# Optimization experiments

Measured on AMD Instinct MI355X. Metric: run time of the kernel, lower is better.

## Reference

```python
import jax, jax.numpy as jnp
import numpy as np
from jax import lax

F8 = jnp.float8_e4m3fn


def setup_inputs() -> dict:
    key = jax.random.key(0)
    kx, kw = jax.random.split(key)
    x = jax.random.normal(kx, (2, 128, 4, 192, 320), dtype=jnp.float32)
    # matches reset_parameters: normal(0, 0.02) then cast to fp8
    weight = jax.random.normal(kw, (128, 128, 3, 3, 3), dtype=jnp.float32) * 0.02
    return {"x": x, "weight": weight}


def reference(x, weight):
    # fp8 e4m3 quantization round-trip (the torch module stores/consumes fp8),
    # compute/accumulate in fp32 as an fp8 conv kernel would.
    xq = x.astype(F8).astype(jnp.float32)
    wq = weight.astype(F8).astype(jnp.float32)
    # causal temporal padding: (kT-1, 0) = (2, 0); spatial 'same' padding (1,1)
    xp = jnp.pad(xq, ((0, 0), (0, 0), (2, 0), (1, 1), (1, 1)))
    out = lax.conv_general_dilated(
        xp, wq,
        window_strides=(1, 1, 1),
        padding='VALID',
        dimension_numbers=('NCDHW', 'OIDHW', 'NCDHW'),
    )  # (B, 128, 4, 192, 320)
    return out
```

## Files before the change

### kernel.cpp

```cpp
#include <hip/hip_runtime.h>
#include <hip/hip_fp8.h>


using f32x16 = __attribute__((ext_vector_type(16))) float;
using i32x8 = __attribute__((ext_vector_type(8))) int;
typedef long long i64;
struct alignas(16) L2v { i64 x, y; };

namespace {
constexpr int Cc = 128, Dd = 4, Hh = 192, Ww = 320;
constexpr int HP = 194, WP = 322;
constexpr int NTAP = 27;
constexpr size_t PLANE = (size_t)4 * WP * 32;
constexpr size_t XQ_BYTES = (size_t)2 * Dd * HP * PLANE;
constexpr int ZA = 8 * 2 * 2576;
constexpr int ZB = 8 * 192 * 32;
constexpr int GSTR = WP * 32;
}

__global__ __launch_bounds__(256) void zero_pad_kernel(unsigned char* __restrict__ xq) {
  int i = blockIdx.x * 256 + threadIdx.x;
  if (i < ZA) {
    int bd = i / (2 * 2576);
    int r = i - bd * (2 * 2576);
    int hsel = r / 2576, seg = r - hsel * 2576;
    L2v z{0, 0};
    *(L2v*)(xq + ((size_t)bd * HP + (hsel ? 193 : 0)) * PLANE + (size_t)seg * 16) = z;
  } else if (i < ZA + ZB) {
    int j = i - ZA;
    int bd = j / (192 * 32);
    int r = j - bd * (192 * 32);
    int h = r / 32 + 1;
    int t = r & 31;
    int g = t >> 3, s2 = t & 7;
    int wsel = s2 >> 2, part = s2 & 3;
    *(i64*)(xq + ((size_t)bd * HP + h) * PLANE + (size_t)g * GSTR
            + (size_t)(wsel ? 321 : 0) * 32 + part * 8) = 0;
  }
}

__global__ __launch_bounds__(256) void qx_kernel(const float* __restrict__ x,
                                                 unsigned char* __restrict__ xq) {
  __shared__ unsigned char lt[64 * 136];
  const int tid = threadIdx.x;
  const int b = blockIdx.z >> 2, d = blockIdx.z & 3;
  const int h = blockIdx.y;
  const int w0 = blockIdx.x * 64;
  const int wl = tid & 63, cig = tid >> 6;
  const size_t cstr = (size_t)Dd * Hh * Ww;
  const float* xp = x + (((size_t)b * Cc * Dd + d) * Hh + h) * Ww + w0 + wl;
  #pragma unroll 4
  for (int i = 0; i < 32; ++i) {
    int ci = cig * 32 + i;
    __hip_fp8_e4m3 q(xp[ci * cstr]);
    lt[wl * 136 + ci] = q.__x;
  }
  __syncthreads();
  unsigned char* plane = xq + ((size_t)(b * Dd + d) * HP + h + 1) * PLANE;
  {
    int g = tid >> 6, w = tid & 63;
    const unsigned char* src = lt + w * 136 + g * 32;
    i64 a0 = *(const i64*)(src), a1 = *(const i64*)(src + 8);
    i64 a2 = *(const i64*)(src + 16), a3 = *(const i64*)(src + 24);
    unsigned char* dst = plane + (size_t)g * GSTR + (size_t)(w0 + 1 + w) * 32;
    *(L2v*)dst = L2v{a0, a1};
    *(L2v*)(dst + 16) = L2v{a2, a3};
  }
}

__global__ void wpack_kernel(const float* __restrict__ w, unsigned char* __restrict__ wpk) {
  int idx = blockIdx.x * 256 + threadIdx.x;
  if (idx >= Cc * Cc * NTAP) return;
  int tap = idx % NTAP;
  int t = idx / NTAP;
  int ci = t % Cc, co = t / Cc;
  int cc = ci >> 6, cq = co >> 5;
  int lane = (((ci >> 5) & 1) << 5) | (co & 31);
  __hip_fp8_e4m3 q(w[idx]);
  wpk[((((size_t)tap * 2 + cc) * 4 + cq) * 64 + lane) * 32 + (ci & 31)] = q.__x;
}

__global__ __launch_bounds__(512, 4) void conv_mfma(const unsigned char* __restrict__ xq,
                                                    const unsigned char* __restrict__ wpk,
                                                    float* __restrict__ out) {
  __shared__ unsigned char lb[16 * 2112];
  const int tid = threadIdx.x;
  const int lane = tid & 63, wv = tid >> 6;
  const int l31 = lane & 31, chalf = lane >> 5;
  const int hr = wv >> 2, ch = wv & 3;
  const int id = blockIdx.x;
  const int xcd = id & 7, j = id >> 3;
  const int h0l = j / 40, rem = j - h0l * 40;
  const int z = rem / 5, wx = rem - z * 5;
  const int b = z >> 2, dout = z & 3;
  const int h0 = (xcd * 12 + h0l) * 2;
  const int w0 = wx * 64;
  const int kdmin = dout >= 2 ? 0 : 2 - dout;

  const unsigned char* bbl[3];
  const unsigned char* bbh[3];
  {
    unsigned char* rbase = lb + (hr * 4 + chalf) * 2112;
    #pragma unroll
    for (int kw = 0; kw < 3; ++kw) {
      int wl = l31 + kw;
      int t = (wl >> 2) & 1;
      bbl[kw] = rbase + 32 * wl + 16 * t;
      bbh[kw] = rbase + 32 * wl + 16 * (1 - t);
    }
  }

  f32x16 acc[2];
  #pragma unroll
  for (int n = 0; n < 2; ++n)
    #pragma unroll
    for (int r = 0; r < 16; ++r) acc[n][r] = 0.f;

  for (int kd = kdmin; kd < 3; ++kd) {
    __syncthreads();
    #pragma unroll
    for (int it = 0; it < 3; ++it) {
      int u = tid + it * 512;
      if (u < 1056) {
        int w = u % 66, rest = u / 66;
        int g = rest & 3, hrow = rest >> 2;
        const unsigned char* src = xq
            + ((size_t)(b * Dd + dout + kd - 2) * HP + h0 + hrow) * PLANE
            + (size_t)g * GSTR + (size_t)(w0 + w) * 32;
        L2v lo = *(const L2v*)src;
        L2v hi = *(const L2v*)(src + 16);
        int t = (w >> 2) & 1;
        unsigned char* base = lb + rest * 2112;
        *(L2v*)(base + (2 * w + t) * 16) = lo;
        *(L2v*)(base + (2 * w + 1 - t) * 16) = hi;
      }
    }
    __syncthreads();
    __builtin_amdgcn_s_setprio(1);
    #pragma unroll
    for (int kh = 0; kh < 3; ++kh)
      #pragma unroll
      for (int cc = 0; cc < 2; ++cc) {
        i32x8 av[3];
        #pragma unroll
        for (int kw = 0; kw < 3; ++kw) {
          const unsigned char* ap = wpk +
              ((((size_t)(kd * 9 + kh * 3 + kw) * 2 + cc) * 4 + ch) * 64 + lane) * 32;
          int4 alo = *(const int4*)ap;
          int4 ahi = *(const int4*)(ap + 16);
          av[kw][0] = alo.x; av[kw][1] = alo.y; av[kw][2] = alo.z; av[kw][3] = alo.w;
          av[kw][4] = ahi.x; av[kw][5] = ahi.y; av[kw][6] = ahi.z; av[kw][7] = ahi.w;
        }
        #pragma unroll
        for (int kw = 0; kw < 3; ++kw)
          #pragma unroll
          for (int nf = 0; nf < 2; ++nf) {
            const int off = (kh * 4 + cc * 2) * 2112 + nf * 1024;
            int4 blo = *(const int4*)(bbl[kw] + off);
            int4 bhi = *(const int4*)(bbh[kw] + off);
            i32x8 bv;
            bv[0] = blo.x; bv[1] = blo.y; bv[2] = blo.z; bv[3] = blo.w;
            bv[4] = bhi.x; bv[5] = bhi.y; bv[6] = bhi.z; bv[7] = bhi.w;
            acc[nf] = __builtin_amdgcn_mfma_scale_f32_32x32x64_f8f6f4(
                av[kw], bv, acc[nf], 0, 0, 0, 127, 0, 127);
          }
      }
    __builtin_amdgcn_s_setprio(0);
  }

  #pragma unroll
  for (int nf = 0; nf < 2; ++nf) {
    int ww = w0 + nf * 32 + l31;
    #pragma unroll
    for (int reg = 0; reg < 16; ++reg) {
      int co = ch * 32 + (reg & 3) + 8 * (reg >> 2) + 4 * chalf;
      out[(((size_t)b * Cc + co) * Dd + dout) * (size_t)(Hh * Ww)
          + (size_t)(h0 + hr) * Ww + ww] = acc[nf][reg];
    }
  }
}

extern "C" void kernel_launch(void* const* d_in, const int* in_sizes, int n_in,
                              void* d_out, int out_size, void* d_ws, size_t ws_size,
                              hipStream_t stream) {
  const float* x = (const float*)d_in[0];
  const float* w = (const float*)d_in[1];
  unsigned char* xq = (unsigned char*)d_ws;
  unsigned char* wpk = xq + XQ_BYTES;
  float* out = (float*)d_out;

  int nz = ZA + ZB;
  zero_pad_kernel<<<(nz + 255) / 256, 256, 0, stream>>>(xq);

  dim3 g1(Ww / 64, Hh, 2 * Dd);
  qx_kernel<<<g1, 256, 0, stream>>>(x, xq);

  int nw = Cc * Cc * NTAP;
  wpack_kernel<<<(nw + 255) / 256, 256, 0, stream>>>(w, wpk);

  conv_mfma<<<dim3(3840), 512, 0, stream>>>(xq, wpk, out);
}
```

Measured before the change: 238.4 us.

## Halve block to 4 waves with 64-channel output tiles per wave and split LDS layout

Each block now runs 256 threads (4 waves), and each wave computes two 32-channel output tiles. Every B fragment read from LDS therefore feeds two MFMAs, which halves LDS B reads per MFMA. The LDS layout changes from interleaved 32-byte pixels with a swizzle to separate low and high 16-byte halves placed HB bytes apart, which removes the swizzle arithmetic. The trade-offs are doubled accumulator registers per wave, fewer threads to stage each input tile, and a possible change in LDS bank-conflict behaviour.

```diff
diff --git a/kernel.cpp b/kernel.cpp
--- a/kernel.cpp
+++ b/kernel.cpp
@@ -16,6 +16,7 @@
 constexpr int ZA = 8 * 2 * 2576;
 constexpr int ZB = 8 * 192 * 32;
 constexpr int GSTR = WP * 32;
+constexpr int HB = 1056;
 }
 
 __global__ __launch_bounds__(256) void zero_pad_kernel(unsigned char* __restrict__ xq) {
@@ -80,14 +81,14 @@
   wpk[((((size_t)tap * 2 + cc) * 4 + cq) * 64 + lane) * 32 + (ci & 31)] = q.__x;
 }
 
-__global__ __launch_bounds__(512, 4) void conv_mfma(const unsigned char* __restrict__ xq,
+__global__ __launch_bounds__(256, 4) void conv_mfma(const unsigned char* __restrict__ xq,
                                                     const unsigned char* __restrict__ wpk,
                                                     float* __restrict__ out) {
-  __shared__ unsigned char lb[16 * 2112];
+  __shared__ unsigned char lb[4 * 4 * 2 * HB];
   const int tid = threadIdx.x;
   const int lane = tid & 63, wv = tid >> 6;
   const int l31 = lane & 31, chalf = lane >> 5;
-  const int hr = wv >> 2, ch = wv & 3;
+  const int hr = wv >> 1, ch = wv & 1;
   const int id = blockIdx.x;
   const int xcd = id & 7, j = id >> 3;
   const int h0l = j / 40, rem = j - h0l * 40;
@@ -97,87 +98,80 @@
   const int w0 = wx * 64;
   const int kdmin = dout >= 2 ? 0 : 2 - dout;
 
-  const unsigned char* bbl[3];
-  const unsigned char* bbh[3];
-  {
-    unsigned char* rbase = lb + (hr * 4 + chalf) * 2112;
+  const unsigned char* bb[3];
+  #pragma unroll
+  for (int kw = 0; kw < 3; ++kw)
+    bb[kw] = lb + (hr * 4 + chalf) * 2 * HB + (l31 + kw) * 16;
+
+  f32x16 acc[2][2];
+  #pragma unroll
+  for (int a = 0; a < 2; ++a)
     #pragma unroll
-    for (int kw = 0; kw < 3; ++kw) {
-      int wl = l31 + kw;
-      int t = (wl >> 2) & 1;
-      bbl[kw] = rbase + 32 * wl + 16 * t;
-      bbh[kw] = rbase + 32 * wl + 16 * (1 - t);
-    }
-  }
-
-  f32x16 acc[2];
-  #pragma unroll
-  for (int n = 0; n < 2; ++n)
-    #pragma unroll
-    for (int r = 0; r < 16; ++r) acc[n][r] = 0.f;
+    for (int n = 0; n < 2; ++n)
+      #pragma unroll
+      for (int r = 0; r < 16; ++r) acc[a][n][r] = 0.f;
 
   for (int kd = kdmin; kd < 3; ++kd) {
     __syncthreads();
-    #pragma unroll
-    for (int it = 0; it < 3; ++it) {
-      int u = tid + it * 512;
-      if (u < 1056) {
-        int w = u % 66, rest = u / 66;
-        int g = rest & 3, hrow = rest >> 2;
-        const unsigned char* src = xq
-            + ((size_t)(b * Dd + dout + kd - 2) * HP + h0 + hrow) * PLANE
-            + (size_t)g * GSTR + (size_t)(w0 + w) * 32;
-        L2v lo = *(const L2v*)src;
-        L2v hi = *(const L2v*)(src + 16);
-        int t = (w >> 2) & 1;
-        unsigned char* base = lb + rest * 2112;
-        *(L2v*)(base + (2 * w + t) * 16) = lo;
-        *(L2v*)(base + (2 * w + 1 - t) * 16) = hi;
-      }
+    for (int u = tid; u < 1056; u += 256) {
+      int w = u % 66, rest = u / 66;
+      int g = rest & 3, hrow = rest >> 2;
+      const unsigned char* src = xq
+          + ((size_t)(b * Dd + dout + kd - 2) * HP + h0 + hrow) * PLANE
+          + (size_t)g * GSTR + (size_t)(w0 + w) * 32;
+      L2v lo = *(const L2v*)src;
+      L2v hi = *(const L2v*)(src + 16);
+      unsigned char* base = lb + (hrow * 4 + g) * 2 * HB + w * 16;
+      *(L2v*)(base) = lo;
+      *(L2v*)(base + HB) = hi;
     }
     __syncthreads();
     __builtin_amdgcn_s_setprio(1);
     #pragma unroll
     for (int kh = 0; kh < 3; ++kh)
       #pragma unroll
-      for (int cc = 0; cc < 2; ++cc) {
-        i32x8 av[3];
+      for (int cc = 0; cc < 2; ++cc)
         #pragma unroll
         for (int kw = 0; kw < 3; ++kw) {
-          const unsigned char* ap = wpk +
-              ((((size_t)(kd * 9 + kh * 3 + kw) * 2 + cc) * 4 + ch) * 64 + lane) * 32;
-          int4 alo = *(const int4*)ap;
-          int4 ahi = *(const int4*)(ap + 16);
-          av[kw][0] = alo.x; av[kw][1] = alo.y; av[kw][2] = alo.z; av[kw][3] = alo.w;
-          av[kw][4] = ahi.x; av[kw][5] = ahi.y; av[kw][6] = ahi.z; av[kw][7] = ahi.w;
-        }
-        #pragma unroll
-        for (int kw = 0; kw < 3; ++kw)
+          i32x8 av[2];
+          #pragma unroll
+          for (int ct = 0; ct < 2; ++ct) {
+            const unsigned char* ap = wpk +
+                ((((size_t)((kd * 9 + kh * 3 + kw) * 2) + cc) * 4 + ch * 2 + ct) * 64 + lane) * 32;
+            int4 alo = *(const int4*)ap;
+            int4 ahi = *(const int4*)(ap + 16);
+            av[ct][0] = alo.x; av[ct][1] = alo.y; av[ct][2] = alo.z; av[ct][3] = alo.w;
+            av[ct][4] = ahi.x; av[ct][5] = ahi.y; av[ct][6] = ahi.z; av[ct][7] = ahi.w;
+          }
           #pragma unroll
           for (int nf = 0; nf < 2; ++nf) {
-            const int off = (kh * 4 + cc * 2) * 2112 + nf * 1024;
-            int4 blo = *(const int4*)(bbl[kw] + off);
-            int4 bhi = *(const int4*)(bbh[kw] + off);
+            const int off = (kh * 4 + cc * 2) * 2 * HB + nf * 32 * 16;
+            int4 blo = *(const int4*)(bb[kw] + off);
+            int4 bhi = *(const int4*)(bb[kw] + off + HB);
             i32x8 bv;
             bv[0] = blo.x; bv[1] = blo.y; bv[2] = blo.z; bv[3] = blo.w;
             bv[4] = bhi.x; bv[5] = bhi.y; bv[6] = bhi.z; bv[7] = bhi.w;
-            acc[nf] = __builtin_amdgcn_mfma_scale_f32_32x32x64_f8f6f4(
-                av[kw], bv, acc[nf], 0, 0, 0, 127, 0, 127);
+            #pragma unroll
+            for (int ct = 0; ct < 2; ++ct)
+              acc[ct][nf] = __builtin_amdgcn_mfma_scale_f32_32x32x64_f8f6f4(
+                  av[ct], bv, acc[ct][nf], 0, 0, 0, 127, 0, 127);
           }
-      }
+        }
     __builtin_amdgcn_s_setprio(0);
   }
 
   #pragma unroll
-  for (int nf = 0; nf < 2; ++nf) {
-    int ww = w0 + nf * 32 + l31;
+  for (int ct = 0; ct < 2; ++ct)
     #pragma unroll
-    for (int reg = 0; reg < 16; ++reg) {
-      int co = ch * 32 + (reg & 3) + 8 * (reg >> 2) + 4 * chalf;
-      out[(((size_t)b * Cc + co) * Dd + dout) * (size_t)(Hh * Ww)
-          + (size_t)(h0 + hr) * Ww + ww] = acc[nf][reg];
+    for (int nf = 0; nf < 2; ++nf) {
+      int ww = w0 + nf * 32 + l31;
+      #pragma unroll
+      for (int reg = 0; reg < 16; ++reg) {
+        int co = ch * 64 + ct * 32 + (reg & 3) + 8 * (reg >> 2) + 4 * chalf;
+        out[(((size_t)b * Cc + co) * Dd + dout) * (size_t)(Hh * Ww)
+            + (size_t)(h0 + hr) * Ww + ww] = acc[ct][nf][reg];
+      }
     }
-  }
 }
 
 extern "C" void kernel_launch(void* const* d_in, const int* in_sizes, int n_in,
@@ -198,5 +192,5 @@
   int nw = Cc * Cc * NTAP;
   wpack_kernel<<<(nw + 255) / 256, 256, 0, stream>>>(w, wpk);
 
-  conv_mfma<<<dim3(3840), 512, 0, stream>>>(xq, wpk, out);
+  conv_mfma<<<dim3(3840), 256, 0, stream>>>(xq, wpk, out);
 }
```

After: 235.4 us. Within noise of the previous version (-1.2%).
